# Optimization experiments

Hardware: AMD Instinct MI355X
Metric: run time of the kernel (lower is better)

The kernel has to match this reference:

```python
import jax, jax.numpy as jnp
import numpy as np
import math

B, S, D, H, FF = 32, 577, 768, 12, 3072
Dh = D // H
EPS = 1e-5


def layer_norm(x, w, b):
    mu = jnp.mean(x, axis=-1, keepdims=True)
    var = jnp.mean(jnp.square(x - mu), axis=-1, keepdims=True)
    return (x - mu) * jax.lax.rsqrt(var + EPS) * w + b


def setup_inputs() -> dict:
    key = jax.random.key(0)
    ks = jax.random.split(key, 12)
    s = 0.02
    return {
        "x": jax.random.normal(ks[0], (B, S, D), dtype=jnp.float32),
        "ln1_w": jnp.ones((D,), jnp.float32),
        "ln1_b": jnp.zeros((D,), jnp.float32),
        # stacked per-head Q/K/V projections (head order matches torch concat order)
        "Wq": jax.random.normal(ks[1], (H, D, Dh), jnp.float32) * s,
        "bq": jnp.zeros((H, Dh), jnp.float32),
        "Wk": jax.random.normal(ks[2], (H, D, Dh), jnp.float32) * s,
        "bk": jnp.zeros((H, Dh), jnp.float32),
        "Wv": jax.random.normal(ks[3], (H, D, Dh), jnp.float32) * s,
        "bv": jnp.zeros((H, Dh), jnp.float32),
        "Wo": jax.random.normal(ks[4], (D, D), jnp.float32) * s,
        "bo": jnp.zeros((D,), jnp.float32),
        "ln2_w": jnp.ones((D,), jnp.float32),
        "ln2_b": jnp.zeros((D,), jnp.float32),
        "W1": jax.random.normal(ks[5], (D, FF), jnp.float32) * s,
        "b1": jnp.zeros((FF,), jnp.float32),
        "W2": jax.random.normal(ks[6], (FF, D), jnp.float32) * s,
        "b2": jnp.zeros((D,), jnp.float32),
    }


def reference(x, ln1_w, ln1_b, Wq, bq, Wk, bk, Wv, bv, Wo, bo, ln2_w, ln2_b, W1, b1, W2, b2):
    # pre-norm attention
    h = layer_norm(x, ln1_w, ln1_b)  # [B,S,D]
    q = jnp.einsum('bsd,hde->bhse', h, Wq) + bq[:, None, :]
    k = jnp.einsum('bsd,hde->bhse', h, Wk) + bk[:, None, :]
    v = jnp.einsum('bsd,hde->bhse', h, Wv) + bv[:, None, :]
    scores = jnp.einsum('bhse,bhte->bhst', q, k) / math.sqrt(Dh)
    probs = jax.nn.softmax(scores, axis=-1)
    ctx = jnp.einsum('bhst,bhte->bhse', probs, v)  # [B,H,S,Dh]
    ctx = ctx.transpose(0, 2, 1, 3).reshape(B, S, H * Dh)  # concat heads
    attn_out = ctx @ Wo + bo
    x = x + attn_out
    # pre-norm MLP (exact GELU, as nn.GELU default)
    h2 = layer_norm(x, ln2_w, ln2_b)
    mlp = jax.nn.gelu(h2 @ W1 + b1, approximate=False) @ W2 + b2
    return x + mlp
```

## Files before the change

kernel.cpp:

```cpp
#include <hip/hip_runtime.h>
#include <hip/hip_bf16.h>
#include <stdint.h>

#define B_ 32
#define S_ 577
#define D_ 768
#define H_ 12
#define FF_ 3072
#define MROWS (B_*S_)

typedef __attribute__((ext_vector_type(8))) short sh8;
typedef __attribute__((ext_vector_type(4))) float f32x4;
typedef __attribute__((ext_vector_type(4))) unsigned short us4;

static __device__ __forceinline__ unsigned short f2b(float f) {
  __hip_bfloat16 h = __float2bfloat16(f);
  return *reinterpret_cast<unsigned short*>(&h);
}
static __device__ __forceinline__ float b2f(unsigned short u) {
  __hip_bfloat16 h;
  *reinterpret_cast<unsigned short*>(&h) = u;
  return __bfloat162float(h);
}

static __device__ __forceinline__ float fast_gelu(float v) {
  const float z = fabsf(v) * 0.70710678118f;
  const float t = __builtin_amdgcn_rcpf(__builtin_fmaf(0.3275911f, z, 1.0f));
  float p = 1.061405429f;
  p = __builtin_fmaf(p, t, -1.453152027f);
  p = __builtin_fmaf(p, t,  1.421413741f);
  p = __builtin_fmaf(p, t, -0.284496736f);
  p = __builtin_fmaf(p, t,  0.254829592f);
  p = p * t;
  const float e = __expf(-z * z);
  const float erf_abs = __builtin_fmaf(-p, e, 1.0f);
  const float erf_v = copysignf(erf_abs, v);
  const float hv = 0.5f * v;
  return __builtin_fmaf(hv, erf_v, hv);
}

#define GLOAD_LDS16(gp, lp) \
  __builtin_amdgcn_global_load_lds((const __attribute__((address_space(1))) unsigned int*)(gp), \
                                   (__attribute__((address_space(3))) unsigned int*)(lp), 16, 0, 0)

__global__ __launch_bounds__(256) void packT64(
    const float* __restrict__ src, unsigned short* __restrict__ dst, int K, int N)
{
  __shared__ unsigned short t[64][65];
  const int tid = threadIdx.x;
  const int c = tid & 63, r4 = tid >> 6;
  const int kb = blockIdx.y * 64, nb = blockIdx.x * 64;
#pragma unroll
  for (int p = 0; p < 16; ++p) {
    const int ko = p * 4 + r4;
    t[c][ko] = f2b(src[(size_t)(kb + ko) * N + nb + c]);
  }
  __syncthreads();
#pragma unroll
  for (int p = 0; p < 16; ++p) {
    const int rr = p * 4 + r4;
    dst[(size_t)(nb + rr) * K + kb + c] = t[rr][c];
  }
}

__global__ __launch_bounds__(256) void packQKV64(
    const float* __restrict__ Wq, const float* __restrict__ Wk, const float* __restrict__ Wv,
    unsigned short* __restrict__ dst)
{
  __shared__ unsigned short t[64][65];
  const int tid = threadIdx.x;
  const int c = tid & 63, r4 = tid >> 6;
  const int kb = blockIdx.x * 64;
  const int h = blockIdx.y;
  const int which = blockIdx.z;
  const float* src = ((which == 0) ? Wq : (which == 1) ? Wk : Wv) + (size_t)h * 768 * 64;
#pragma unroll
  for (int p = 0; p < 16; ++p) {
    const int ko = p * 4 + r4;
    t[c][ko] = f2b(src[(size_t)(kb + ko) * 64 + c]);
  }
  __syncthreads();
  unsigned short* db = dst + (size_t)(which * 768 + h * 64) * 768;
#pragma unroll
  for (int p = 0; p < 16; ++p) {
    const int rr = p * 4 + r4;
    db[(size_t)rr * 768 + kb + c] = t[rr][c];
  }
}

__global__ __launch_bounds__(256) void bias_pack(
    const float* __restrict__ bq, const float* __restrict__ bk, const float* __restrict__ bv,
    float* __restrict__ biasq)
{
  const int idx = blockIdx.x * 256 + threadIdx.x;
  if (idx < 2304) {
    const int wb = idx / 768, rb = idx - wb * 768;
    const float* bb = (wb == 0) ? bq : (wb == 1) ? bk : bv;
    biasq[idx] = bb[rb];
  }
}

__global__ __launch_bounds__(256) void ln_bf16(
    const float* __restrict__ x, const float* __restrict__ w, const float* __restrict__ bse,
    unsigned short* __restrict__ out)
{
  const int row = blockIdx.x;
  const int tid = threadIdx.x;
  const float* xr = x + (size_t)row * 768;
  float v0 = xr[tid], v1 = xr[tid + 256], v2 = xr[tid + 512];
  float s = v0 + v1 + v2;
  float ss = v0 * v0 + v1 * v1 + v2 * v2;
#pragma unroll
  for (int off = 32; off >= 1; off >>= 1) {
    s  += __shfl_xor(s, off);
    ss += __shfl_xor(ss, off);
  }
  __shared__ float red[8];
  const int wv = tid >> 6, ln = tid & 63;
  if (ln == 0) { red[wv] = s; red[wv + 4] = ss; }
  __syncthreads();
  s  = red[0] + red[1] + red[2] + red[3];
  ss = red[4] + red[5] + red[6] + red[7];
  const float mu = s * (1.f / 768.f);
  const float var = ss * (1.f / 768.f) - mu * mu;
  const float rs = rsqrtf(var + 1e-5f);
  unsigned short* orow = out + (size_t)row * 768;
  orow[tid]       = f2b((v0 - mu) * rs * w[tid]       + bse[tid]);
  orow[tid + 256] = f2b((v1 - mu) * rs * w[tid + 256] + bse[tid + 256]);
  orow[tid + 512] = f2b((v2 - mu) * rs * w[tid + 512] + bse[tid + 512]);
}

template<int EPI>
__global__ __launch_bounds__(256, 3) void gemm128(
    const unsigned short* __restrict__ A, const unsigned short* __restrict__ Bt,
    const float* __restrict__ bias, const float* __restrict__ res,
    unsigned short* __restrict__ obf, float* __restrict__ of32,
    int M, int N, int K)
{
  __shared__ __align__(16) unsigned short sAB[2][128 * 64];
  const int tid = threadIdx.x;
  const int wid = tid >> 6, ln = tid & 63;
  const int wr = wid >> 1, wc = wid & 1;
  const int l15 = ln & 15, lg = ln >> 4;
  const int l7 = l15 & 7;
  const int uo0 = ((lg) ^ l7) * 8;
  const int uo1 = ((4 + lg) ^ l7) * 8;
  const int srow = ln >> 3;
  const int scol = ((ln & 7) ^ srow) * 8;
  const int NT = K >> 6;

  const int gx = N >> 7;
  const int nwg = gridDim.x;
  const int q = nwg >> 3, r = nwg & 7;
  const int x = blockIdx.x & 7, ii = blockIdx.x >> 3;
  const int wg = (x < r ? x * (q + 1) : r * (q + 1) + (x - r) * q) + ii;
  const int bm = wg / gx, bn = wg - bm * gx;

  const int arow = wr * 64 + l15;
  const int brow = wc * 64 + l15;

  f32x4 acc[4][4] = {};

  for (int t = 0; t < NT; ++t) {
    const int kt = t * 64;
    __syncthreads();
#pragma unroll
    for (int j = 0; j < 4; ++j) {
      const int idx = wid * 4 + j;
      int ga = bm * 128 + idx * 8 + srow; if (ga >= M) ga = M - 1;
      GLOAD_LDS16(A + (size_t)ga * K + kt + scol, sAB[0] + idx * 512);
    }
#pragma unroll
    for (int j = 0; j < 4; ++j) {
      const int idx = wid * 4 + j;
      const int gb = bn * 128 + idx * 8 + srow;
      GLOAD_LDS16(Bt + (size_t)gb * K + kt + scol, sAB[1] + idx * 512);
    }
    asm volatile("s_waitcnt vmcnt(0)" ::: "memory");
    __syncthreads();

#pragma unroll
    for (int kk = 0; kk < 2; ++kk) {
      const int uo = kk ? uo1 : uo0;
      sh8 af[4], bf[4];
#pragma unroll
      for (int mi = 0; mi < 4; ++mi)
        af[mi] = *(const sh8*)(sAB[0] + (arow + mi * 16) * 64 + uo);
#pragma unroll
      for (int ni = 0; ni < 4; ++ni)
        bf[ni] = *(const sh8*)(sAB[1] + (brow + ni * 16) * 64 + uo);
#pragma unroll
      for (int mi = 0; mi < 4; ++mi)
#pragma unroll
        for (int ni = 0; ni < 4; ++ni)
          acc[mi][ni] = __builtin_amdgcn_mfma_f32_16x16x32_bf16(af[mi], bf[ni], acc[mi][ni], 0, 0, 0);
    }
  }

  constexpr int ESTR = 132;
  float* eps = (float*)sAB;
#pragma unroll
  for (int pass = 0; pass < 4; ++pass) {
    __syncthreads();
    if (wr == (pass >> 1)) {
      const int mib = (pass & 1) * 2;
#pragma unroll
      for (int ml = 0; ml < 2; ++ml)
#pragma unroll
        for (int ni = 0; ni < 4; ++ni)
#pragma unroll
          for (int rr = 0; rr < 4; ++rr)
            eps[(ml * 16 + lg * 4 + rr) * ESTR + wc * 64 + ni * 16 + l15] = acc[mib + ml][ni][rr];
    }
    __syncthreads();
#pragma unroll
    for (int pp = 0; pp < 4; ++pp) {
      const int idx = pp * 256 + tid;
      const int rl = idx >> 5;
      const int c4 = (idx & 31) * 4;
      const int grow = bm * 128 + pass * 32 + rl;
      if (grow < M) {
        f32x4 v = *(const f32x4*)(eps + rl * ESTR + c4);
        const int gcol = bn * 128 + c4;
        const f32x4 bv = *(const f32x4*)(bias + gcol);
        v += bv;
        if (EPI == 2) {
#pragma unroll
          for (int e = 0; e < 4; ++e) v[e] = fast_gelu(v[e]);
        }
        if (EPI == 1) {
          const f32x4 rv = *(const f32x4*)(res + (size_t)grow * N + gcol);
          v += rv;
          *(f32x4*)(of32 + (size_t)grow * N + gcol) = v;
        } else {
          us4 o = { f2b(v[0]), f2b(v[1]), f2b(v[2]), f2b(v[3]) };
          *(us4*)(obf + (size_t)grow * N + gcol) = o;
        }
      }
    }
  }
}

__global__ __launch_bounds__(256) void attn(
    const unsigned short* __restrict__ qkv, unsigned short* __restrict__ ctx)
{
  constexpr int KP = 72;
  __shared__ __align__(16) unsigned short sQ[64 * KP];
  __shared__ __align__(16) unsigned short sK[64 * KP];
  __shared__ __align__(16) unsigned short sVT[64 * KP];
  __shared__ __align__(16) unsigned short sP[4][16 * KP];
  const int tid = threadIdx.x, wv = tid >> 6, ln = tid & 63;
  const int l15 = ln & 15, lg = ln >> 4;
  const int b = blockIdx.z, h = blockIdx.y, qt = blockIdx.x;
  const size_t base = (size_t)b * S_ * 2304 + h * 64;
  const unsigned short* qp = qkv + base;
  const unsigned short* kp = qkv + base + 768;
  const unsigned short* vp = qkv + base + 1536;

  {
    const int r = tid >> 2, c = (tid & 3) * 16;
    int row = qt * 64 + r; if (row >= S_) row = S_ - 1;
    const unsigned short* g = qp + (size_t)row * 2304 + c;
#pragma unroll
    for (int half = 0; half < 2; ++half) {
      sh8 v = *(const sh8*)(g + half * 8);
      unsigned short o[8];
#pragma unroll
      for (int j = 0; j < 8; ++j) o[j] = f2b(b2f((unsigned short)v[j]) * 0.125f);
      *(sh8*)(sQ + r * KP + c + half * 8) = *(sh8*)o;
    }
  }

  f32x4 oacc[4] = {};
  float m_run = -1e30f, l_run = 0.f;
  const int nt = (S_ + 63) / 64;
  for (int t = 0; t < nt; ++t) {
    __syncthreads();
    {
      const int r = tid >> 2, c = (tid & 3) * 16;
      int row = t * 64 + r; if (row >= S_) row = S_ - 1;
      const unsigned short* g = kp + (size_t)row * 2304 + c;
      *(sh8*)(sK + r * KP + c)     = *(const sh8*)g;
      *(sh8*)(sK + r * KP + c + 8) = *(const sh8*)(g + 8);
    }
#pragma unroll
    for (int uu = 0; uu < 2; ++uu) {
      const int u = tid + uu * 256;
      const int e = u & 63, kvb = u >> 6;
      unsigned short val[8];
#pragma unroll
      for (int j = 0; j < 8; ++j) {
        int row = t * 64 + kvb * 8 + j; if (row >= S_) row = S_ - 1;
        val[j] = vp[(size_t)row * 2304 + e];
      }
      *(sh8*)(sVT + e * KP + kvb * 8) = *(sh8*)val;
    }
    __syncthreads();

    f32x4 sacc[4] = {};
#pragma unroll
    for (int kk = 0; kk < 2; ++kk) {
      sh8 bq = *(const sh8*)(sQ + (wv * 16 + l15) * KP + kk * 32 + lg * 8);
#pragma unroll
      for (int f = 0; f < 4; ++f) {
        sh8 ak = *(const sh8*)(sK + (f * 16 + l15) * KP + kk * 32 + lg * 8);
        sacc[f] = __builtin_amdgcn_mfma_f32_16x16x32_bf16(ak, bq, sacc[f], 0, 0, 0);
      }
    }

    float sv[4][4];
    float pmax = -1e30f;
#pragma unroll
    for (int f = 0; f < 4; ++f)
#pragma unroll
      for (int r = 0; r < 4; ++r) {
        const int kva = t * 64 + f * 16 + lg * 4 + r;
        float sc = sacc[f][r];
        if (kva >= S_) sc = -1e30f;
        sv[f][r] = sc;
        pmax = fmaxf(pmax, sc);
      }
    pmax = fmaxf(pmax, __shfl_xor(pmax, 16));
    pmax = fmaxf(pmax, __shfl_xor(pmax, 32));
    const float mnew = fmaxf(m_run, pmax);
    const float alpha = __expf(m_run - mnew);
    float psum = 0.f;
    unsigned short pb[4][4];
#pragma unroll
    for (int f = 0; f < 4; ++f)
#pragma unroll
      for (int r = 0; r < 4; ++r) {
        const float p = __expf(sv[f][r] - mnew);
        psum += p;
        pb[f][r] = f2b(p);
      }
    psum += __shfl_xor(psum, 16);
    psum += __shfl_xor(psum, 32);
    l_run = l_run * alpha + psum;
    m_run = mnew;
#pragma unroll
    for (int f = 0; f < 4; ++f) {
      oacc[f][0] *= alpha; oacc[f][1] *= alpha;
      oacc[f][2] *= alpha; oacc[f][3] *= alpha;
    }
#pragma unroll
    for (int f = 0; f < 4; ++f) {
      us4 pk = { pb[f][0], pb[f][1], pb[f][2], pb[f][3] };
      *(us4*)(sP[wv] + l15 * KP + f * 16 + lg * 4) = pk;
    }
    __syncthreads();

#pragma unroll
    for (int kk = 0; kk < 2; ++kk) {
      sh8 bp = *(const sh8*)(sP[wv] + l15 * KP + kk * 32 + lg * 8);
#pragma unroll
      for (int fe = 0; fe < 4; ++fe) {
        sh8 av = *(const sh8*)(sVT + (fe * 16 + l15) * KP + kk * 32 + lg * 8);
        oacc[fe] = __builtin_amdgcn_mfma_f32_16x16x32_bf16(av, bp, oacc[fe], 0, 0, 0);
      }
    }
  }

  const int qa = qt * 64 + wv * 16 + l15;
  if (qa < S_) {
    const float inv = 1.f / l_run;
    const size_t orow = ((size_t)b * S_ + qa) * 768 + h * 64;
#pragma unroll
    for (int fe = 0; fe < 4; ++fe) {
      unsigned short pk[4];
#pragma unroll
      for (int r = 0; r < 4; ++r) pk[r] = f2b(oacc[fe][r] * inv);
      *(us4*)(ctx + orow + fe * 16 + lg * 4) = *(us4*)pk;
    }
  }
}

extern "C" void kernel_launch(void* const* d_in, const int* in_sizes, int n_in,
                              void* d_out, int out_size, void* d_ws, size_t ws_size,
                              hipStream_t stream)
{
  const float* x    = (const float*)d_in[0];
  const float* ln1w = (const float*)d_in[1];
  const float* ln1b = (const float*)d_in[2];
  const float* Wq   = (const float*)d_in[3];
  const float* bq   = (const float*)d_in[4];
  const float* Wk   = (const float*)d_in[5];
  const float* bk   = (const float*)d_in[6];
  const float* Wv   = (const float*)d_in[7];
  const float* bv   = (const float*)d_in[8];
  const float* Wo   = (const float*)d_in[9];
  const float* bo   = (const float*)d_in[10];
  const float* ln2w = (const float*)d_in[11];
  const float* ln2b = (const float*)d_in[12];
  const float* W1   = (const float*)d_in[13];
  const float* b1   = (const float*)d_in[14];
  const float* W2   = (const float*)d_in[15];
  const float* b2   = (const float*)d_in[16];
  float* out = (float*)d_out;
  char* ws = (char*)d_ws;

  unsigned short* wqkvT = (unsigned short*)(ws + 0);
  unsigned short* woT   = (unsigned short*)(ws + 3538944);
  unsigned short* w1T   = (unsigned short*)(ws + 4718592);
  unsigned short* w2T   = (unsigned short*)(ws + 9437184);
  float*          biasq = (float*)(ws + 14155776);
  unsigned short* hbf   = (unsigned short*)(ws + 14164992);
  unsigned short* qkvb  = (unsigned short*)(ws + 42525696);
  unsigned short* ctxb  = (unsigned short*)(ws + 127607808);
  unsigned short* mlp1  = qkvb;

  packQKV64<<<dim3(12, 12, 3), 256, 0, stream>>>(Wq, Wk, Wv, wqkvT);
  bias_pack<<<9, 256, 0, stream>>>(bq, bk, bv, biasq);
  packT64<<<dim3(12, 12), 256, 0, stream>>>(Wo, woT, 768, 768);
  packT64<<<dim3(48, 12), 256, 0, stream>>>(W1, w1T, 768, 3072);
  packT64<<<dim3(12, 48), 256, 0, stream>>>(W2, w2T, 3072, 768);

  ln_bf16<<<MROWS, 256, 0, stream>>>(x, ln1w, ln1b, hbf);
  gemm128<0><<<145 * 18, 256, 0, stream>>>(hbf, wqkvT, biasq, nullptr, qkvb, nullptr,
                                           MROWS, 2304, 768);
  attn<<<dim3(10, 12, 32), 256, 0, stream>>>(qkvb, ctxb);
  gemm128<1><<<145 * 6, 256, 0, stream>>>(ctxb, woT, bo, x, nullptr, out,
                                          MROWS, 768, 768);
  ln_bf16<<<MROWS, 256, 0, stream>>>(out, ln2w, ln2b, hbf);
  gemm128<2><<<145 * 24, 256, 0, stream>>>(hbf, w1T, b1, nullptr, mlp1, nullptr,
                                           MROWS, 3072, 768);
  gemm128<1><<<145 * 6, 256, 0, stream>>>(mlp1, w2T, b2, out, nullptr, out,
                                          MROWS, 768, 3072);
}
```

Before: 493.8 us.

## Double attention query tile to 128 rows, fold softmax scale into Wq

The attention kernel now runs 512 threads (8 waves) per block over 128 query rows. Each K/V tile loaded into shared memory is therefore reused by twice as many queries, and the grid is halved. The 1/sqrt(Dh) scale is folded into the packed Wq weights and bias, removing per-element rescaling when Q is loaded. Row clamping and score masking now apply only to the last KV tile. In exchange, shared memory and register use per block rise and there are fewer blocks to spread across CUs.

```diff
diff --git a/kernel.cpp b/kernel.cpp
--- a/kernel.cpp
+++ b/kernel.cpp
@@ -74,10 +74,11 @@
   const int h = blockIdx.y;
   const int which = blockIdx.z;
   const float* src = ((which == 0) ? Wq : (which == 1) ? Wk : Wv) + (size_t)h * 768 * 64;
+  const float scl = (which == 0) ? 0.125f : 1.0f;
 #pragma unroll
   for (int p = 0; p < 16; ++p) {
     const int ko = p * 4 + r4;
-    t[c][ko] = f2b(src[(size_t)(kb + ko) * 64 + c]);
+    t[c][ko] = f2b(src[(size_t)(kb + ko) * 64 + c] * scl);
   }
   __syncthreads();
   unsigned short* db = dst + (size_t)(which * 768 + h * 64) * 768;
@@ -96,7 +97,7 @@
   if (idx < 2304) {
     const int wb = idx / 768, rb = idx - wb * 768;
     const float* bb = (wb == 0) ? bq : (wb == 1) ? bk : bv;
-    biasq[idx] = bb[rb];
+    biasq[idx] = bb[rb] * (wb == 0 ? 0.125f : 1.0f);
   }
 }
 
@@ -241,14 +242,14 @@
   }
 }
 
-__global__ __launch_bounds__(256) void attn(
+__global__ __launch_bounds__(512) void attn(
     const unsigned short* __restrict__ qkv, unsigned short* __restrict__ ctx)
 {
   constexpr int KP = 72;
-  __shared__ __align__(16) unsigned short sQ[64 * KP];
+  __shared__ __align__(16) unsigned short sQ[128 * KP];
   __shared__ __align__(16) unsigned short sK[64 * KP];
   __shared__ __align__(16) unsigned short sVT[64 * KP];
-  __shared__ __align__(16) unsigned short sP[4][16 * KP];
+  __shared__ __align__(16) unsigned short sP[8][16 * KP];
   const int tid = threadIdx.x, wv = tid >> 6, ln = tid & 63;
   const int l15 = ln & 15, lg = ln >> 4;
   const int b = blockIdx.z, h = blockIdx.y, qt = blockIdx.x;
@@ -259,16 +260,10 @@
 
   {
     const int r = tid >> 2, c = (tid & 3) * 16;
-    int row = qt * 64 + r; if (row >= S_) row = S_ - 1;
+    int row = qt * 128 + r; if (row >= S_) row = S_ - 1;
     const unsigned short* g = qp + (size_t)row * 2304 + c;
-#pragma unroll
-    for (int half = 0; half < 2; ++half) {
-      sh8 v = *(const sh8*)(g + half * 8);
-      unsigned short o[8];
-#pragma unroll
-      for (int j = 0; j < 8; ++j) o[j] = f2b(b2f((unsigned short)v[j]) * 0.125f);
-      *(sh8*)(sQ + r * KP + c + half * 8) = *(sh8*)o;
-    }
+    *(sh8*)(sQ + r * KP + c)     = *(const sh8*)g;
+    *(sh8*)(sQ + r * KP + c + 8) = *(const sh8*)(g + 8);
   }
 
   f32x4 oacc[4] = {};
@@ -276,24 +271,35 @@
   const int nt = (S_ + 63) / 64;
   for (int t = 0; t < nt; ++t) {
     __syncthreads();
-    {
-      const int r = tid >> 2, c = (tid & 3) * 16;
-      int row = t * 64 + r; if (row >= S_) row = S_ - 1;
-      const unsigned short* g = kp + (size_t)row * 2304 + c;
-      *(sh8*)(sK + r * KP + c)     = *(const sh8*)g;
-      *(sh8*)(sK + r * KP + c + 8) = *(const sh8*)(g + 8);
-    }
-#pragma unroll
-    for (int uu = 0; uu < 2; ++uu) {
-      const int u = tid + uu * 256;
-      const int e = u & 63, kvb = u >> 6;
-      unsigned short val[8];
-#pragma unroll
-      for (int j = 0; j < 8; ++j) {
-        int row = t * 64 + kvb * 8 + j; if (row >= S_) row = S_ - 1;
-        val[j] = vp[(size_t)row * 2304 + e];
-      }
-      *(sh8*)(sVT + e * KP + kvb * 8) = *(sh8*)val;
+    if (t < nt - 1) {
+      {
+        const int r = tid >> 3, c = (tid & 7) * 8;
+        *(sh8*)(sK + r * KP + c) = *(const sh8*)(kp + (size_t)(t * 64 + r) * 2304 + c);
+      }
+      {
+        const int e = tid & 63, kvb = tid >> 6;
+        const unsigned short* vb = vp + (size_t)(t * 64 + kvb * 8) * 2304 + e;
+        unsigned short val[8];
+#pragma unroll
+        for (int j = 0; j < 8; ++j) val[j] = vb[(size_t)j * 2304];
+        *(sh8*)(sVT + e * KP + kvb * 8) = *(sh8*)val;
+      }
+    } else {
+      {
+        const int r = tid >> 3, c = (tid & 7) * 8;
+        int row = t * 64 + r; if (row >= S_) row = S_ - 1;
+        *(sh8*)(sK + r * KP + c) = *(const sh8*)(kp + (size_t)row * 2304 + c);
+      }
+      {
+        const int e = tid & 63, kvb = tid >> 6;
+        unsigned short val[8];
+#pragma unroll
+        for (int j = 0; j < 8; ++j) {
+          int row = t * 64 + kvb * 8 + j; if (row >= S_) row = S_ - 1;
+          val[j] = vp[(size_t)row * 2304 + e];
+        }
+        *(sh8*)(sVT + e * KP + kvb * 8) = *(sh8*)val;
+      }
     }
     __syncthreads();
 
@@ -308,18 +314,18 @@
       }
     }
 
-    float sv[4][4];
+    if (t == nt - 1) {
+#pragma unroll
+      for (int f = 0; f < 4; ++f)
+#pragma unroll
+        for (int r = 0; r < 4; ++r)
+          if (t * 64 + f * 16 + lg * 4 + r >= S_) sacc[f][r] = -1e30f;
+    }
     float pmax = -1e30f;
 #pragma unroll
     for (int f = 0; f < 4; ++f)
 #pragma unroll
-      for (int r = 0; r < 4; ++r) {
-        const int kva = t * 64 + f * 16 + lg * 4 + r;
-        float sc = sacc[f][r];
-        if (kva >= S_) sc = -1e30f;
-        sv[f][r] = sc;
-        pmax = fmaxf(pmax, sc);
-      }
+      for (int r = 0; r < 4; ++r) pmax = fmaxf(pmax, sacc[f][r]);
     pmax = fmaxf(pmax, __shfl_xor(pmax, 16));
     pmax = fmaxf(pmax, __shfl_xor(pmax, 32));
     const float mnew = fmaxf(m_run, pmax);
@@ -330,7 +336,7 @@
     for (int f = 0; f < 4; ++f)
 #pragma unroll
       for (int r = 0; r < 4; ++r) {
-        const float p = __expf(sv[f][r] - mnew);
+        const float p = __expf(sacc[f][r] - mnew);
         psum += p;
         pb[f][r] = f2b(p);
       }
@@ -361,7 +367,7 @@
     }
   }
 
-  const int qa = qt * 64 + wv * 16 + l15;
+  const int qa = qt * 128 + wv * 16 + l15;
   if (qa < S_) {
     const float inv = 1.f / l_run;
     const size_t orow = ((size_t)b * S_ + qa) * 768 + h * 64;
@@ -418,7 +424,7 @@
   ln_bf16<<<MROWS, 256, 0, stream>>>(x, ln1w, ln1b, hbf);
   gemm128<0><<<145 * 18, 256, 0, stream>>>(hbf, wqkvT, biasq, nullptr, qkvb, nullptr,
                                            MROWS, 2304, 768);
-  attn<<<dim3(10, 12, 32), 256, 0, stream>>>(qkvb, ctxb);
+  attn<<<dim3(5, 12, 32), 512, 0, stream>>>(qkvb, ctxb);
   gemm128<1><<<145 * 6, 256, 0, stream>>>(ctxb, woT, bo, x, nullptr, out,
                                           MROWS, 768, 768);
   ln_bf16<<<MROWS, 256, 0, stream>>>(out, ln2w, ln2b, hbf);
```

Result: no change. 484.5 us (-1.9%).
